# Kernel tuning notes

Measured on AMD Instinct MI355X. Metric: run time of the kernel, lower is better.

Reference implementation:

```python
import jax, jax.numpy as jnp
import numpy as np

VOCAB_SIZE = 13
EMBED_DIM = 50
HIDDEN_DIM = 50
BATCH = 2048
SEQ_LEN = 2048


def setup_inputs() -> dict:
    key = jax.random.key(0)
    ks = jax.random.split(key, 10)
    s = 0.1
    return {
        "x": jax.random.randint(ks[0], (BATCH, SEQ_LEN), 0, VOCAB_SIZE),
        "embed": jax.random.normal(ks[1], (VOCAB_SIZE, EMBED_DIM), jnp.float32),
        "W_ih": jax.random.normal(ks[2], (4 * HIDDEN_DIM, EMBED_DIM), jnp.float32) * s,
        "W_hh": jax.random.normal(ks[3], (4 * HIDDEN_DIM, HIDDEN_DIM), jnp.float32) * s,
        "b_ih": jax.random.normal(ks[4], (4 * HIDDEN_DIM,), jnp.float32) * s,
        "b_hh": jax.random.normal(ks[5], (4 * HIDDEN_DIM,), jnp.float32) * s,
        "W1": jax.random.normal(ks[6], (HIDDEN_DIM, HIDDEN_DIM), jnp.float32) * s,
        "b1": jax.random.normal(ks[7], (HIDDEN_DIM,), jnp.float32) * s,
        "W2": jax.random.normal(ks[8], (1, HIDDEN_DIM), jnp.float32) * s,
        "b2": jax.random.normal(ks[9], (1,), jnp.float32) * s,
    }


def reference(x, embed, W_ih, W_hh, b_ih, b_hh, W1, b1, W2, b2):
    B = x.shape[0]
    H = HIDDEN_DIM
    embeds = embed[x]                    # [B, T, E]
    xs = jnp.swapaxes(embeds, 0, 1)      # [T, B, E] for scan over time

    def step(carry, xt):
        hx, cx = carry
        gates = xt @ W_ih.T + b_ih + hx @ W_hh.T + b_hh   # [B, 4H]
        i = jax.nn.sigmoid(gates[:, 0 * H:1 * H])
        f = jax.nn.sigmoid(gates[:, 1 * H:2 * H])
        g = jnp.tanh(gates[:, 2 * H:3 * H])
        o = jax.nn.sigmoid(gates[:, 3 * H:4 * H])
        cx = f * cx + i * g
        hx = o * jnp.tanh(cx)
        return (hx, cx), None

    init = (jnp.zeros((B, H), embeds.dtype), jnp.zeros((B, H), embeds.dtype))
    (hx, _), _ = jax.lax.scan(step, init, xs)

    h = jax.nn.relu(hx @ W1.T + b1)
    out = (h @ W2.T + b2).squeeze(1)     # [B]
    return out
```

## Files before the change

### kernel.cpp

```cpp
#include <hip/hip_runtime.h>
#include <hip/hip_fp16.h>

#define T_SEQ 2048
#define HID   50
#define KP    64
#define MB    8
#define NBLK  256
#define NTHR  512
#define HSTR  80
#define BUFB  (MB*HSTR)

#define NLOG2E  1.4426950408889634f
#define N2LOG2E 2.8853900817779268f

typedef __attribute__((ext_vector_type(8))) _Float16 half8;
typedef __attribute__((ext_vector_type(4))) float    f32x4;

__device__ __forceinline__ ushort f16b(float f){ return __half_as_ushort(__float2half(f)); }
__device__ __forceinline__ float rcp_(float x){ return __builtin_amdgcn_rcpf(x); }
__device__ __forceinline__ float ex2_(float x){ return __builtin_amdgcn_exp2f(x); }
__device__ __forceinline__ float dpp_swap8(float v){
    return __int_as_float(__builtin_amdgcn_mov_dpp(__float_as_int(v), 0x128, 0xF, 0xF, true));
}

__global__ void build_B(const float* __restrict__ embed, const float* __restrict__ Wih,
                        const float* __restrict__ Whh, const float* __restrict__ bih,
                        const float* __restrict__ bhh, ushort* __restrict__ Bm) {
    int idx = blockIdx.x * blockDim.x + threadIdx.x;
    if (idx >= 256 * KP) return;
    int col = idx >> 6, k = idx & 63;
    int w = col >> 5, j = (col >> 4) & 1, cc = col & 15;
    int g = 2 * j + (cc >> 3);
    int u = 8 * w + (cc & 7);
    ushort v = 0;
    if (u < HID) {
        int r = g * HID + u;
        float s = (g == 2) ? -N2LOG2E : -NLOG2E;
        if (k < HID) {
            v = f16b(s * Whh[r * HID + k]);
        } else if (k < 63) {
            float t = 0.f;
            for (int e = 0; e < HID; ++e)
                t = fmaf(embed[(k - 50) * HID + e], Wih[r * HID + e], t);
            v = f16b(s * t);
        } else {
            v = f16b(s * (bih[r] + bhh[r]));
        }
    }
    Bm[idx] = v;
}

__global__ __launch_bounds__(NTHR, 2) void lstm8w(
    const int*    __restrict__ x,
    const ushort* __restrict__ Bm,
    const float*  __restrict__ W1,
    const float*  __restrict__ b1,
    const float*  __restrict__ W2,
    const float*  __restrict__ b2,
    float*        __restrict__ out)
{
    const int t    = threadIdx.x;
    const int w    = t >> 6;
    const int l    = t & 63;
    const int q    = l >> 4;
    const int c16  = l & 15;
    const bool lo  = (c16 < 8);
    const int u    = 8 * w + (c16 & 7);
    const int myrow = 2 * q + (lo ? 0 : 1);

    __shared__ __align__(16) ushort hbuf[2 * BUFB];
    __shared__ __align__(16) unsigned char tokL[MB * T_SEQ];
    __shared__ float zb[HID * MB];

    half8 bf[2][2];
    {
        const ushort* bp = Bm + (w * 32 + c16) * KP + q * 8;
        #pragma unroll
        for (int j = 0; j < 2; ++j) {
            bf[j][0] = *(const half8*)(bp + j * 16 * KP);
            bf[j][1] = *(const half8*)(bp + j * 16 * KP + 32);
        }
    }
    asm volatile("" : "+v"(bf[0][0]), "+v"(bf[0][1]), "+v"(bf[1][0]), "+v"(bf[1][1]));

    {
        const int4* xs = (const int4*)(x + (long)blockIdx.x * MB * T_SEQ);
        for (int i = t; i < MB * T_SEQ / 4; i += NTHR) {
            int4 v = xs[i];
            uint pk = (uint)(v.x & 0xFF) | ((uint)(v.y & 0xFF) << 8) |
                      ((uint)(v.z & 0xFF) << 16) | ((uint)(v.w & 0xFF) << 24);
            *(uint*)(tokL + i * 4) = pk;
        }
    }
    for (int i = t; i < 2 * BUFB; i += NTHR) hbuf[i] = 0;
    __syncthreads();

    int tk0 = tokL[w * T_SEQ + 0];
    int tk1 = tokL[w * T_SEQ + 1];
    if (l == 0) {
        hbuf[0 * BUFB + w * HSTR + 63] = 0x3C00;
        hbuf[1 * BUFB + w * HSTR + 63] = 0x3C00;
        hbuf[0 * BUFB + w * HSTR + 50 + tk0] = 0x3C00;
        hbuf[1 * BUFB + w * HSTR + 50 + tk1] = 0x3C00;
    }
    int t0r = tk1, t1r = tk0, t2r = tk1;
    __syncthreads();

    const ushort* ar  = hbuf + (c16 >> 1) * HSTR + q * 8;
    ushort*       wr_ = hbuf + myrow * HSTR + u;
    const unsigned char* tp = tokL + w * T_SEQ;

    float cs = 0.f;

#define MFMA_(A,B,C) __builtin_amdgcn_mfma_f32_16x16x32_f16((A),(B),(C),0,0,0)
#define STEP(P) do {                                                              \
        int it = step + 2 + (P); if (it > T_SEQ - 1) it = T_SEQ - 1;              \
        int tn = tp[it];                                  \
        half8 a0 = *(const half8*)(ar + (P) * BUFB);                              \
        half8 a1 = *(const half8*)(ar + (P) * BUFB + 32);                         \
        const f32x4 zz = {0.f, 0.f, 0.f, 0.f};                                    \
        __builtin_amdgcn_s_setprio(1);                                            \
        f32x4 z0a = MFMA_(a0, bf[0][0], zz);    \
        f32x4 z0b = MFMA_(a1, bf[0][1], zz);                                      \
        f32x4 z1a = MFMA_(a0, bf[1][0], zz);                                      \
        f32x4 z1b = MFMA_(a1, bf[1][1], zz);                                      \
        __builtin_amdgcn_s_setprio(0);                                            \
        float s0l = z0a[0] + z0b[0];                     \
        float s0h = z0a[2] + z0b[2];                     \
        float s1l = z1a[0] + z1b[0];                     \
        float s1h = z1a[2] + z1b[2];                     \
        float rx0 = dpp_swap8(lo ? s0h : s0l);    \
        float rx1 = dpp_swap8(lo ? s1h : s1l);                                    \
        float gi = lo ? s0l : rx0;                  \
        float gf = lo ? rx0 : s0h;                                                \
        float gg = lo ? s1l : rx1;                                                \
        float go = lo ? rx1 : s1h;                                                \
                        \
        float pi = ex2_(fminf(gi, 30.f));                                         \
        float pf = ex2_(fminf(gf, 30.f));                                         \
        float qg = ex2_(fminf(gg, 30.f));                                         \
        float Df = 1.f + pf;                                                      \
        float D2 = (1.f + pi) * (1.f + qg);                                       \
        float ivA = rcp_(Df * D2);                                                \
        float fv  = ivA * D2;                                       \
        float igs = ivA * Df * fmaf(N2LOG2E, qg, -N2LOG2E);      \
        cs = fmaf(fv, cs, igs);                                                   \
        float po = ex2_(fminf(go, 30.f));                                         \
        float qc = ex2_(fminf(cs, 30.f));                       \
        float ivB = rcp_((1.f + po) * (1.f + qc));                                \
        float hh  = ivB * (1.f - qc);                       \
        if (u < HID) wr_[(1 - (P)) * BUFB] = f16b(hh);                            \
        if (l == 0) {                                                             \
            ushort* hb = hbuf + (1 - (P)) * BUFB + w * HSTR + 50;                 \
            hb[t0r] = 0;                                                          \
            hb[t2r] = 0x3C00;                                                     \
        }                                                                         \
        t0r = t1r; t1r = t2r; t2r = tn;                                           \
        __syncthreads();                                                          \
    } while (0)

    #pragma unroll 1
    for (int step = 0; step < T_SEQ; step += 2) {
        STEP(0);
        STEP(1);
    }
#undef STEP
#undef MFMA_

    if (t < MB * HID) {
        int m = t & 7, uu = t >> 3;
        float a = b1[uu];
        const ushort* hr = hbuf + m * HSTR;
        #pragma unroll 10
        for (int k = 0; k < HID; ++k)
            a = fmaf(W1[uu * HID + k], __half2float(__ushort_as_half(hr[k])), a);
        zb[uu * MB + m] = fmaxf(a, 0.f);
    }
    __syncthreads();
    if (t < MB) {
        float a = b2[0];
        #pragma unroll 10
        for (int j = 0; j < HID; ++j)
            a = fmaf(W2[j], zb[j * MB + t], a);
        out[blockIdx.x * MB + t] = a;
    }
}

extern "C" void kernel_launch(void* const* d_in, const int* in_sizes, int n_in,
                              void* d_out, int out_size, void* d_ws, size_t ws_size,
                              hipStream_t stream) {
    const int*   x     = (const int*)  d_in[0];
    const float* embed = (const float*)d_in[1];
    const float* W_ih  = (const float*)d_in[2];
    const float* W_hh  = (const float*)d_in[3];
    const float* b_ih  = (const float*)d_in[4];
    const float* b_hh  = (const float*)d_in[5];
    const float* W1    = (const float*)d_in[6];
    const float* b1    = (const float*)d_in[7];
    const float* W2    = (const float*)d_in[8];
    const float* b2    = (const float*)d_in[9];
    float* out = (float*)d_out;

    ushort* Bm = (ushort*)d_ws;

    build_B<<<(256 * KP + 255) / 256, 256, 0, stream>>>(
        embed, W_ih, W_hh, b_ih, b_hh, Bm);

    lstm8w<<<NBLK, NTHR, 0, stream>>>(
        x, Bm, W1, b1, W2, b2, out);
}
```

Before: 748.3 us.

## Read tokens from global via scalar loads, chain MFMA accumulation, drop gate clamps

The kernel no longer stages each block's token sequence into a 16 KB shared-memory byte buffer. Each wave instead reads its token straight from global memory every step, using a wave-uniform row pointer so the load can go through the scalar path, and that load is issued two steps ahead. The two K-half MFMAs per gate pair now accumulate into one register instead of being summed with separate adds, which drops some VALU work but makes the two MFMAs serially dependent. The fminf clamps before exp2 are removed on the gate inputs (kept only on the cell state). This trims the per-step critical path, at the risk of inf/NaN if gate pre-activations grow large.

```diff
diff --git a/kernel.cpp b/kernel.cpp
--- a/kernel.cpp
+++ b/kernel.cpp
@@ -67,9 +67,9 @@
     const bool lo  = (c16 < 8);
     const int u    = 8 * w + (c16 & 7);
     const int myrow = 2 * q + (lo ? 0 : 1);
+    const int wu   = __builtin_amdgcn_readfirstlane(w);
 
     __shared__ __align__(16) ushort hbuf[2 * BUFB];
-    __shared__ __align__(16) unsigned char tokL[MB * T_SEQ];
     __shared__ float zb[HID * MB];
 
     half8 bf[2][2];
@@ -83,79 +83,71 @@
     }
     asm volatile("" : "+v"(bf[0][0]), "+v"(bf[0][1]), "+v"(bf[1][0]), "+v"(bf[1][1]));
 
-    {
-        const int4* xs = (const int4*)(x + (long)blockIdx.x * MB * T_SEQ);
-        for (int i = t; i < MB * T_SEQ / 4; i += NTHR) {
-            int4 v = xs[i];
-            uint pk = (uint)(v.x & 0xFF) | ((uint)(v.y & 0xFF) << 8) |
-                      ((uint)(v.z & 0xFF) << 16) | ((uint)(v.w & 0xFF) << 24);
-            *(uint*)(tokL + i * 4) = pk;
-        }
-    }
     for (int i = t; i < 2 * BUFB; i += NTHR) hbuf[i] = 0;
+
+    const int* xw = x + ((long)blockIdx.x * MB + wu) * T_SEQ;
+    int tk0 = xw[0];
+    int tk1 = xw[1];
     __syncthreads();
-
-    int tk0 = tokL[w * T_SEQ + 0];
-    int tk1 = tokL[w * T_SEQ + 1];
     if (l == 0) {
-        hbuf[0 * BUFB + w * HSTR + 63] = 0x3C00;
-        hbuf[1 * BUFB + w * HSTR + 63] = 0x3C00;
-        hbuf[0 * BUFB + w * HSTR + 50 + tk0] = 0x3C00;
-        hbuf[1 * BUFB + w * HSTR + 50 + tk1] = 0x3C00;
+        hbuf[0 * BUFB + wu * HSTR + 63] = 0x3C00;
+        hbuf[1 * BUFB + wu * HSTR + 63] = 0x3C00;
+        hbuf[0 * BUFB + wu * HSTR + 50 + tk0] = 0x3C00;
+        hbuf[1 * BUFB + wu * HSTR + 50 + tk1] = 0x3C00;
     }
     int t0r = tk1, t1r = tk0, t2r = tk1;
     __syncthreads();
 
     const ushort* ar  = hbuf + (c16 >> 1) * HSTR + q * 8;
     ushort*       wr_ = hbuf + myrow * HSTR + u;
-    const unsigned char* tp = tokL + w * T_SEQ;
+    ushort*       hbw = hbuf + wu * HSTR + 50;
 
     float cs = 0.f;
 
 #define MFMA_(A,B,C) __builtin_amdgcn_mfma_f32_16x16x32_f16((A),(B),(C),0,0,0)
 #define STEP(P) do {                                                              \
         int it = step + 2 + (P); if (it > T_SEQ - 1) it = T_SEQ - 1;              \
-        int tn = tp[it];                                  \
+        int tn = xw[it];                             \
         half8 a0 = *(const half8*)(ar + (P) * BUFB);                              \
         half8 a1 = *(const half8*)(ar + (P) * BUFB + 32);                         \
         const f32x4 zz = {0.f, 0.f, 0.f, 0.f};                                    \
         __builtin_amdgcn_s_setprio(1);                                            \
-        f32x4 z0a = MFMA_(a0, bf[0][0], zz);    \
-        f32x4 z0b = MFMA_(a1, bf[0][1], zz);                                      \
-        f32x4 z1a = MFMA_(a0, bf[1][0], zz);                                      \
-        f32x4 z1b = MFMA_(a1, bf[1][1], zz);                                      \
+        f32x4 z0 = MFMA_(a0, bf[0][0], zz);                                       \
+        z0 = MFMA_(a1, bf[0][1], z0);              \
+        f32x4 z1 = MFMA_(a0, bf[1][0], zz);                                       \
+        z1 = MFMA_(a1, bf[1][1], z1);                                             \
         __builtin_amdgcn_s_setprio(0);                                            \
-        float s0l = z0a[0] + z0b[0];                     \
-        float s0h = z0a[2] + z0b[2];                     \
-        float s1l = z1a[0] + z1b[0];                     \
-        float s1h = z1a[2] + z1b[2];                     \
+        float s0l = z0[0];                               \
+        float s0h = z0[2];                               \
+        float s1l = z1[0];                               \
+        float s1h = z1[2];                               \
         float rx0 = dpp_swap8(lo ? s0h : s0l);    \
         float rx1 = dpp_swap8(lo ? s1h : s1l);                                    \
         float gi = lo ? s0l : rx0;                  \
         float gf = lo ? rx0 : s0h;                                                \
         float gg = lo ? s1l : rx1;                                                \
         float go = lo ? rx1 : s1h;                                                \
-                        \
-        float pi = ex2_(fminf(gi, 30.f));                                         \
-        float pf = ex2_(fminf(gf, 30.f));                                         \
-        float qg = ex2_(fminf(gg, 30.f));                                         \
+               \
+        float pi = ex2_(gi);                                                      \
+        float pf = ex2_(gf);                                                      \
+        float qg = ex2_(gg);                                                      \
         float Df = 1.f + pf;                                                      \
         float D2 = (1.f + pi) * (1.f + qg);                                       \
         float ivA = rcp_(Df * D2);                                                \
         float fv  = ivA * D2;                                       \
         float igs = ivA * Df * fmaf(N2LOG2E, qg, -N2LOG2E);      \
         cs = fmaf(fv, cs, igs);                                                   \
-        float po = ex2_(fminf(go, 30.f));                                         \
-        float qc = ex2_(fminf(cs, 30.f));                       \
+        float po = ex2_(go);                                                      \
+        float qc = ex2_(fminf(cs, 30.f));       \
         float ivB = rcp_((1.f + po) * (1.f + qc));                                \
         float hh  = ivB * (1.f - qc);                       \
         if (u < HID) wr_[(1 - (P)) * BUFB] = f16b(hh);                            \
         if (l == 0) {                                                             \
-            ushort* hb = hbuf + (1 - (P)) * BUFB + w * HSTR + 50;                 \
+            ushort* hb = hbw + (1 - (P)) * BUFB;                                  \
             hb[t0r] = 0;                                                          \
             hb[t2r] = 0x3C00;                                                     \
         }                                                                         \
-        t0r = t1r; t1r = t2r; t2r = tn;                                           \
+        t0r = t1r; t1r = t2r; t2r = tn;                          \
         __syncthreads();                                                          \
     } while (0)
 
```

Result: faster. 703.9 us (-5.9%).
